# Kernel optimization log

Measured on AMD Instinct MI355X. Metric: run time of the kernel, lower is better.

Reference implementation:

```python
import jax, jax.numpy as jnp
import numpy as np

N = 100000   # nodes
E = 1200000  # edges
G = 512      # graphs in batch
H = 64       # hidden_dim
EED = 8      # edge_emb_dim
VOCABS = (120, 10, 7, 5, 2)
EDIMS = (64, 16, 8, 8, 4)
BN_EPS = 1e-5


def _lin(x, w, b):
    # torch nn.Linear: y = x @ W^T + b
    return x @ w.T + b


def setup_inputs() -> dict:
    key = jax.random.key(0)
    ks = iter(jax.random.split(key, 64))
    s = 0.02
    d = {}
    d["x"] = jax.random.randint(next(ks), (N, 5), 0, 120)
    d["edge_index"] = jax.random.randint(next(ks), (2, E), 0, N)
    d["edge_attr"] = jax.random.randint(next(ks), (E, 3), 0, 16)
    d["batch"] = jnp.sort(jax.random.randint(next(ks), (N,), 0, G))
    for i, (v, dd) in enumerate(zip(VOCABS, EDIMS)):
        d[f"emb{i}"] = jax.random.normal(next(ks), (v, dd), jnp.float32) * s
    d["proj_w"] = jax.random.normal(next(ks), (H, sum(EDIMS)), jnp.float32) * s
    d["proj_b"] = jnp.zeros((H,), jnp.float32)
    for i in (1, 2, 3):
        d[f"eemb{i}"] = jax.random.normal(next(ks), (16, EED), jnp.float32) * s
        d[f"lin_e{i}_w"] = jax.random.normal(next(ks), (H, EED), jnp.float32) * s
        d[f"lin_e{i}_b"] = jnp.zeros((H,), jnp.float32)
        d[f"eps{i}"] = jnp.zeros((), jnp.float32)
        d[f"mlp{i}_w1"] = jax.random.normal(next(ks), (H, H), jnp.float32) * s
        d[f"mlp{i}_b1"] = jnp.zeros((H,), jnp.float32)
        d[f"mlp{i}_w2"] = jax.random.normal(next(ks), (H, H), jnp.float32) * s
        d[f"mlp{i}_b2"] = jnp.zeros((H,), jnp.float32)
    d["bn_g"] = jnp.ones((H,), jnp.float32)
    d["bn_b"] = jnp.zeros((H,), jnp.float32)
    d["bn_rm"] = jnp.zeros((H,), jnp.float32)
    d["bn_rv"] = jnp.ones((H,), jnp.float32)
    d["gate_w"] = jax.random.normal(next(ks), (1, H), jnp.float32) * s
    d["gate_b"] = jnp.zeros((1,), jnp.float32)
    d["head_w1"] = jax.random.normal(next(ks), (128, H), jnp.float32) * s
    d["head_b1"] = jnp.zeros((128,), jnp.float32)
    d["head_w2"] = jax.random.normal(next(ks), (1, 128), jnp.float32) * s
    d["head_b2"] = jnp.zeros((1,), jnp.float32)
    return d


def reference(x, edge_index, edge_attr, batch,
              emb0, emb1, emb2, emb3, emb4, proj_w, proj_b,
              eemb1, lin_e1_w, lin_e1_b, eps1, mlp1_w1, mlp1_b1, mlp1_w2, mlp1_b2,
              eemb2, lin_e2_w, lin_e2_b, eps2, mlp2_w1, mlp2_b1, mlp2_w2, mlp2_b2,
              eemb3, lin_e3_w, lin_e3_b, eps3, mlp3_w1, mlp3_b1, mlp3_w2, mlp3_b2,
              bn_g, bn_b, bn_rm, bn_rv, gate_w, gate_b,
              head_w1, head_b1, head_w2, head_b2):
    # --- node embedding lookup (clamped per-table, as in torch) ---
    tabs = [emb0, emb1, emb2, emb3, emb4]
    feats = [t[jnp.clip(x[:, i], 0, t.shape[0] - 1)] for i, t in enumerate(tabs)]
    h = jnp.concatenate(feats, axis=-1)            # [N, 100]
    h = _lin(h, proj_w, proj_b)                    # [N, H]  (dropout = identity, eval)

    # --- edge hash, shared by all blocks ---
    eh = (edge_attr[:, 0] + 3 * edge_attr[:, 1] + 7 * edge_attr[:, 2]) % 16  # [E]
    src, dst = edge_index[0], edge_index[1]

    def gine(h, eemb, lw, lb, eps, w1, b1, w2, b2):
        # GINEConv: mlp((1+eps) x_i + sum_j relu(x_j + lin(e_ij)))
        e = _lin(eemb[eh], lw, lb)                        # [E, H]
        msg = jax.nn.relu(h[src] + e)                     # [E, H] gather + combine
        agg = jax.ops.segment_sum(msg, dst, num_segments=N)  # scatter-add to targets
        z = (1.0 + eps) * h + agg
        return _lin(jax.nn.relu(_lin(z, w1, b1)), w2, b2)

    h = jax.nn.relu(gine(h, eemb1, lin_e1_w, lin_e1_b, eps1, mlp1_w1, mlp1_b1, mlp1_w2, mlp1_b2))
    h = jax.nn.relu(gine(h, eemb2, lin_e2_w, lin_e2_b, eps2, mlp2_w1, mlp2_b1, mlp2_w2, mlp2_b2))
    h = jax.nn.relu(gine(h, eemb3, lin_e3_w, lin_e3_b, eps3, mlp3_w1, mlp3_b1, mlp3_w2, mlp3_b2))

    # BatchNorm1d (eval mode, running stats)
    h = (h - bn_rm) * jax.lax.rsqrt(bn_rv + BN_EPS) * bn_g + bn_b

    # AttentionalAggregation: segment softmax over gate, weighted segment sum
    gate = _lin(h, gate_w, gate_b)[:, 0]                  # [N]
    m = jax.ops.segment_max(gate, batch, num_segments=G)  # [G]
    w = jnp.exp(gate - m[batch])
    den = jax.ops.segment_sum(w, batch, num_segments=G) + 1e-16
    alpha = w / den[batch]                                # [N]
    graph = jax.ops.segment_sum(alpha[:, None] * h, batch, num_segments=G)  # [G, H]

    out = _lin(jax.nn.relu(_lin(graph, head_w1, head_b1)), head_w2, head_b2)  # [G, 1]
    return out[:, 0]
```

## Files before the change

kernel.cpp:

```cpp
#include <hip/hip_runtime.h>
#include <stdint.h>

#define N_NODES 100000
#define N_EDGES 1200000
#define N_GRAPH 512
#define HID 64

#define NBUCK 391
#define BCAP  4096
#define CHUNK 4096

#define PRE_W0  (144 * 64 + 3 * 1024 + 64 + NBUCK)
#define PRE_JOBS (PRE_W0 + 6 * 4096)

typedef __attribute__((ext_vector_type(8))) short bshort8;
typedef __attribute__((ext_vector_type(4))) float f32x4;

__device__ __forceinline__ unsigned short f2bf(float f) {
    unsigned u = __float_as_uint(f);
    u += 0x7FFF + ((u >> 16) & 1);
    return (unsigned short)(u >> 16);
}
__device__ __forceinline__ float bf2f(unsigned short b) {
    return __uint_as_float((unsigned)b << 16);
}

__global__ __launch_bounds__(256) void k_pre(
    const float* emb0, const float* emb1, const float* emb2, const float* emb3, const float* emb4,
    const float* proj_w,
    const float* ee1, const float* lw1, const float* lb1,
    const float* ee2, const float* lw2, const float* lb2,
    const float* ee3, const float* lw3, const float* lb3,
    const float* bn_g, const float* bn_b, const float* bn_rm, const float* bn_rv,
    const float* w11, const float* w12, const float* w21, const float* w22,
    const float* w31, const float* w32,
    float* ptab, float* elin, float* bnsc, float* bnsh, int* cursor,
    unsigned short* wbf)
{
    int job = blockIdx.x * 256 + threadIdx.x;
    if (job < 144 * 64) {
        int row = job >> 6, c = job & 63;
        const float* emb; int lr, dim, off;
        if (row < 120)      { emb = emb0; lr = row;       dim = 64; off = 0;  }
        else if (row < 130) { emb = emb1; lr = row - 120; dim = 16; off = 64; }
        else if (row < 137) { emb = emb2; lr = row - 130; dim = 8;  off = 80; }
        else if (row < 142) { emb = emb3; lr = row - 137; dim = 8;  off = 88; }
        else                { emb = emb4; lr = row - 142; dim = 4;  off = 96; }
        float s = 0.f;
        for (int d = 0; d < dim; ++d)
            s += emb[lr * dim + d] * proj_w[c * 100 + off + d];
        ptab[row * 64 + c] = s;
    } else if (job < 144 * 64 + 3 * 1024) {
        int j = job - 144 * 64;
        int L = j >> 10; int r = (j >> 6) & 15; int c = j & 63;
        const float* ee = (L == 0) ? ee1 : (L == 1) ? ee2 : ee3;
        const float* lw = (L == 0) ? lw1 : (L == 1) ? lw2 : lw3;
        const float* lb = (L == 0) ? lb1 : (L == 1) ? lb2 : lb3;
        float s = lb[c];
        for (int d = 0; d < 8; ++d) s += ee[r * 8 + d] * lw[c * 8 + d];
        elin[j] = s;
    } else if (job < 144 * 64 + 3 * 1024 + 64) {
        int c = job - (144 * 64 + 3 * 1024);
        float sc = bn_g[c] * rsqrtf(bn_rv[c] + 1e-5f);
        bnsc[c] = sc;
        bnsh[c] = bn_b[c] - bn_rm[c] * sc;
    } else if (job < PRE_W0) {
        cursor[job - (144 * 64 + 3 * 1024 + 64)] = 0;
    } else if (job < PRE_JOBS) {
        int j2 = job - PRE_W0;
        int sel = j2 >> 12;
        const float* W = (sel == 0) ? w11 : (sel == 1) ? w12 : (sel == 2) ? w21
                       : (sel == 3) ? w22 : (sel == 4) ? w31 : w32;
        wbf[j2] = f2bf(W[j2 & 4095]);
    }
}

__global__ __launch_bounds__(256) void k_embed(const int* x, const float* ptab,
                                               const float* proj_b, unsigned short* h2) {
    int id = blockIdx.x * 256 + threadIdx.x;
    if (id >= N_NODES * HID) return;
    int n = id >> 6, c = id & 63;
    const int* xr = x + n * 5;
    int r0 = min(max(xr[0], 0), 119);
    int r1 = 120 + min(max(xr[1], 0), 9);
    int r2 = 130 + min(max(xr[2], 0), 6);
    int r3 = 137 + min(max(xr[3], 0), 4);
    int r4 = 142 + min(max(xr[4], 0), 1);
    float v = proj_b[c] + ptab[r0 * 64 + c] + ptab[r1 * 64 + c] + ptab[r2 * 64 + c]
            + ptab[r3 * 64 + c] + ptab[r4 * 64 + c];
    h2[id] = f2bf(v);
}

__global__ __launch_bounds__(256) void k_gptr(const int* batch, int* gptr) {
    int n = blockIdx.x * 256 + threadIdx.x;
    if (n >= N_NODES) return;
    int b = batch[n];
    int bp = (n == 0) ? -1 : batch[n - 1];
    for (int g = bp + 1; g <= b; ++g) gptr[g] = n;
    if (n == N_NODES - 1) {
        for (int g = b + 1; g <= N_GRAPH; ++g) gptr[g] = N_NODES;
    }
}

__global__ __launch_bounds__(256) void k_bin(const int* __restrict__ ei,
                                             const int* __restrict__ ea,
                                             int* __restrict__ cursor,
                                             int* __restrict__ binned) {
    __shared__ int pay[CHUNK];
    __shared__ unsigned short bkid[CHUNK];
    __shared__ int hist[NBUCK], inc[NBUCK], tmp[NBUCK], gdelta[NBUCK];
    int t = threadIdx.x;
    int e0 = blockIdx.x * CHUNK;
    for (int i = t; i < NBUCK; i += 256) hist[i] = 0;
    __syncthreads();
    int mypay[16], myrb[16];
    #pragma unroll
    for (int j = 0; j < 16; ++j) {
        int e = e0 + j * 256 + t;
        myrb[j] = -1;
        if (e < N_EDGES) {
            int s = ei[e];
            int d = ei[N_EDGES + e];
            int hsh = (ea[e * 3] + 3 * ea[e * 3 + 1] + 7 * ea[e * 3 + 2]) & 15;
            int b = d >> 8;
            mypay[j] = s | (hsh << 17) | ((d & 255) << 21);
            int r = atomicAdd(&hist[b], 1);
            myrb[j] = r | (b << 12);
        }
    }
    __syncthreads();
    for (int i = t; i < NBUCK; i += 256) inc[i] = hist[i];
    __syncthreads();
    for (int off = 1; off < NBUCK; off <<= 1) {
        for (int i = t; i < NBUCK; i += 256) tmp[i] = inc[i] + ((i >= off) ? inc[i - off] : 0);
        __syncthreads();
        for (int i = t; i < NBUCK; i += 256) inc[i] = tmp[i];
        __syncthreads();
    }
    for (int i = t; i < NBUCK; i += 256) {
        int c = hist[i];
        int gp = c ? atomicAdd(&cursor[i], c) : 0;
        gdelta[i] = i * BCAP + gp - (inc[i] - c);
    }
    __syncthreads();
    #pragma unroll
    for (int j = 0; j < 16; ++j) {
        if (myrb[j] >= 0) {
            int b = myrb[j] >> 12, r = myrb[j] & 0xFFF;
            int slot = (inc[b] - hist[b]) + r;
            pay[slot] = mypay[j];
            bkid[slot] = (unsigned short)b;
        }
    }
    __syncthreads();
    int tot = inc[NBUCK - 1];
    for (int i = t; i < tot; i += 256)
        binned[gdelta[bkid[i]] + i] = pay[i];
}

__global__ __launch_bounds__(512) void k_bscan(const int* cursor, int* bbase, int* rowptr) {
    __shared__ int s[512], tp[512];
    int t = threadIdx.x;
    int v = (t < NBUCK) ? cursor[t] : 0;
    s[t] = v;
    __syncthreads();
    for (int off = 1; off < 512; off <<= 1) {
        tp[t] = s[t] + ((t >= off) ? s[t - off] : 0);
        __syncthreads();
        s[t] = tp[t];
        __syncthreads();
    }
    if (t < NBUCK) bbase[t] = s[t] - v;
    if (t == 0) { bbase[NBUCK] = N_EDGES; rowptr[N_NODES] = N_EDGES; }
}

__global__ __launch_bounds__(256) void k_fin(const int* __restrict__ binned,
                                             const int* __restrict__ cursor,
                                             const int* __restrict__ bbase,
                                             int* __restrict__ rowptr,
                                             int* __restrict__ epk) {
    __shared__ int h2[256], sc[256], cur[256];
    int b = blockIdx.x, t = threadIdx.x;
    int cnt = cursor[b];
    int gb = bbase[b];
    int node0 = b << 8;
    h2[t] = 0;
    __syncthreads();
    const int* bp = binned + b * BCAP;
    for (int i = t; i < cnt; i += 256) atomicAdd(&h2[(bp[i] >> 21) & 255], 1);
    __syncthreads();
    sc[t] = h2[t];
    __syncthreads();
    for (int off = 1; off < 256; off <<= 1) {
        int v = (t >= off) ? sc[t - off] : 0;
        __syncthreads();
        sc[t] += v;
        __syncthreads();
    }
    int ex = sc[t] - h2[t];
    cur[t] = ex;
    int n = node0 + t;
    if (n < N_NODES) rowptr[n] = gb + ex;
    __syncthreads();
    for (int i = t; i < cnt; i += 256) {
        int p = bp[i];
        int pos = atomicAdd(&cur[(p >> 21) & 255], 1);
        epk[gb + pos] = p & 0x1FFFFF;
    }
}

__global__ __launch_bounds__(256) void k_gather(const unsigned short* __restrict__ h2,
                                                const float* __restrict__ elinL,
                                                const int* __restrict__ rowptr,
                                                const int* __restrict__ epk,
                                                float* __restrict__ agg) {
    __shared__ float es[16 * 64];
    int t = threadIdx.x;
    ((float4*)es)[t] = ((const float4*)elinL)[t];
    __syncthreads();
    int n = blockIdx.x * 4 + (t >> 6);
    if (n >= N_NODES) return;
    int lane = t & 63;
    int grp = lane >> 4;
    int c4 = (lane & 15) << 2;
    int p0 = rowptr[n], p1 = rowptr[n + 1];
    int deg = p1 - p0;
    int nb = min(deg, 64);
    int pkv = (lane < deg) ? epk[p0 + lane] : 0;
    float4 acc = make_float4(0.f, 0.f, 0.f, 0.f);
    #pragma unroll
    for (int j = 0; j < 8; ++j) {
        int e = grp + j * 4;
        if (e < nb) {
            int pk = __shfl(pkv, e, 64);
            ushort4 a = *(const ushort4*)(h2 + (pk & 0x1FFFF) * 64 + c4);
            float4 ev = *(const float4*)(es + ((pk >> 17) & 15) * 64 + c4);
            acc.x += fmaxf(bf2f(a.x) + ev.x, 0.f);
            acc.y += fmaxf(bf2f(a.y) + ev.y, 0.f);
            acc.z += fmaxf(bf2f(a.z) + ev.z, 0.f);
            acc.w += fmaxf(bf2f(a.w) + ev.w, 0.f);
        }
    }
    for (int e = grp + 32; e < nb; e += 4) {
        int pk = __shfl(pkv, e, 64);
        ushort4 a = *(const ushort4*)(h2 + (pk & 0x1FFFF) * 64 + c4);
        float4 ev = *(const float4*)(es + ((pk >> 17) & 15) * 64 + c4);
        acc.x += fmaxf(bf2f(a.x) + ev.x, 0.f);
        acc.y += fmaxf(bf2f(a.y) + ev.y, 0.f);
        acc.z += fmaxf(bf2f(a.z) + ev.z, 0.f);
        acc.w += fmaxf(bf2f(a.w) + ev.w, 0.f);
    }
    for (int p = p0 + 64 + grp; p < p1; p += 4) {
        int pk = epk[p];
        ushort4 a = *(const ushort4*)(h2 + (pk & 0x1FFFF) * 64 + c4);
        float4 ev = *(const float4*)(es + ((pk >> 17) & 15) * 64 + c4);
        acc.x += fmaxf(bf2f(a.x) + ev.x, 0.f);
        acc.y += fmaxf(bf2f(a.y) + ev.y, 0.f);
        acc.z += fmaxf(bf2f(a.z) + ev.z, 0.f);
        acc.w += fmaxf(bf2f(a.w) + ev.w, 0.f);
    }
    acc.x += __shfl_down(acc.x, 32, 64);
    acc.y += __shfl_down(acc.y, 32, 64);
    acc.z += __shfl_down(acc.z, 32, 64);
    acc.w += __shfl_down(acc.w, 32, 64);
    acc.x += __shfl_down(acc.x, 16, 64);
    acc.y += __shfl_down(acc.y, 16, 64);
    acc.z += __shfl_down(acc.z, 16, 64);
    acc.w += __shfl_down(acc.w, 16, 64);
    if (grp == 0) *(float4*)(agg + n * 64 + c4) = acc;
}

__global__ __launch_bounds__(256) void k_mlpm(const unsigned short* __restrict__ h2in,
                                              const float* __restrict__ agg,
                                              const float* __restrict__ epsp,
                                              const unsigned short* __restrict__ wbf1,
                                              const float* __restrict__ b1,
                                              const unsigned short* __restrict__ wbf2,
                                              const float* __restrict__ b2,
                                              unsigned short* __restrict__ h2out,
                                              const float* __restrict__ bnsc,
                                              const float* __restrict__ bnsh,
                                              const float* __restrict__ gate_w,
                                              const float* __restrict__ gate_b,
                                              float* __restrict__ gate) {
    __shared__ unsigned short zb[64 * 72];
    __shared__ unsigned short hb[64 * 72];
    int t = threadIdx.x;
    int row0 = blockIdx.x * 64;
    float epsv = 1.f + epsp[0];
    for (int idx = t; idx < 1024; idx += 256) {
        int r = idx >> 4, c4 = (idx & 15) << 2;
        int gr = row0 + r;
        ushort4 zv = {0, 0, 0, 0};
        if (gr < N_NODES) {
            ushort4 a = *(const ushort4*)(h2in + gr * 64 + c4);
            float4 b = *(const float4*)(agg + gr * 64 + c4);
            zv.x = f2bf(epsv * bf2f(a.x) + b.x);
            zv.y = f2bf(epsv * bf2f(a.y) + b.y);
            zv.z = f2bf(epsv * bf2f(a.z) + b.z);
            zv.w = f2bf(epsv * bf2f(a.w) + b.w);
        }
        *(ushort4*)(zb + r * 72 + c4) = zv;
    }
    int lane = t & 63, wv = t >> 6;
    int quad = lane >> 4, lc = lane & 15;
    int m0 = wv * 16;
    bshort8 w1f[4][2];
    #pragma unroll
    for (int nt = 0; nt < 4; ++nt)
        #pragma unroll
        for (int kt = 0; kt < 2; ++kt)
            w1f[nt][kt] = *(const bshort8*)(wbf1 + (nt * 16 + lc) * 64 + kt * 32 + quad * 8);
    bshort8 w2f[4][2];
    #pragma unroll
    for (int nt = 0; nt < 4; ++nt)
        #pragma unroll
        for (int kt = 0; kt < 2; ++kt)
            w2f[nt][kt] = *(const bshort8*)(wbf2 + (nt * 16 + lc) * 64 + kt * 32 + quad * 8);
    __syncthreads();
    bshort8 a0 = *(const bshort8*)(zb + (m0 + lc) * 72 + quad * 8);
    bshort8 a1 = *(const bshort8*)(zb + (m0 + lc) * 72 + 32 + quad * 8);
    f32x4 acc1[4];
    #pragma unroll
    for (int nt = 0; nt < 4; ++nt) {
        acc1[nt] = (f32x4){0.f, 0.f, 0.f, 0.f};
        acc1[nt] = __builtin_amdgcn_mfma_f32_16x16x32_bf16(a0, w1f[nt][0], acc1[nt], 0, 0, 0);
        acc1[nt] = __builtin_amdgcn_mfma_f32_16x16x32_bf16(a1, w1f[nt][1], acc1[nt], 0, 0, 0);
    }
    #pragma unroll
    for (int nt = 0; nt < 4; ++nt) {
        float bb = b1[nt * 16 + lc];
        #pragma unroll
        for (int reg = 0; reg < 4; ++reg) {
            float v = fmaxf(acc1[nt][reg] + bb, 0.f);
            hb[(m0 + quad * 4 + reg) * 72 + nt * 16 + lc] = f2bf(v);
        }
    }
    bshort8 c0 = *(const bshort8*)(hb + (m0 + lc) * 72 + quad * 8);
    bshort8 c1 = *(const bshort8*)(hb + (m0 + lc) * 72 + 32 + quad * 8);
    f32x4 acc2[4];
    #pragma unroll
    for (int nt = 0; nt < 4; ++nt) {
        acc2[nt] = (f32x4){0.f, 0.f, 0.f, 0.f};
        acc2[nt] = __builtin_amdgcn_mfma_f32_16x16x32_bf16(c0, w2f[nt][0], acc2[nt], 0, 0, 0);
        acc2[nt] = __builtin_amdgcn_mfma_f32_16x16x32_bf16(c1, w2f[nt][1], acc2[nt], 0, 0, 0);
    }
    if (gate == nullptr) {
        #pragma unroll
        for (int reg = 0; reg < 4; ++reg) {
            int gr = row0 + m0 + quad * 4 + reg;
            if (gr < N_NODES) {
                #pragma unroll
                for (int nt = 0; nt < 4; ++nt) {
                    int col = nt * 16 + lc;
                    float v = fmaxf(acc2[nt][reg] + b2[col], 0.f);
                    h2out[gr * 64 + col] = f2bf(v);
                }
            }
        }
    } else {
        float gb = gate_b[0];
        #pragma unroll
        for (int reg = 0; reg < 4; ++reg) {
            int gr = row0 + m0 + quad * 4 + reg;
            float p = 0.f;
            #pragma unroll
            for (int nt = 0; nt < 4; ++nt) {
                int col = nt * 16 + lc;
                float v = fmaxf(acc2[nt][reg] + b2[col], 0.f) * bnsc[col] + bnsh[col];
                p += v * gate_w[col];
                if (gr < N_NODES) h2out[gr * 64 + col] = f2bf(v);
            }
            p += __shfl_down(p, 8, 16);
            p += __shfl_down(p, 4, 16);
            p += __shfl_down(p, 2, 16);
            p += __shfl_down(p, 1, 16);
            if (lc == 0 && gr < N_NODES) gate[gr] = p + gb;
        }
    }
}

__global__ __launch_bounds__(256) void k_att(const unsigned short* __restrict__ h2,
                                             const float* __restrict__ gate,
                                             const int* __restrict__ gptr,
                                             const float* __restrict__ hw1,
                                             const float* __restrict__ hb1,
                                             const float* __restrict__ hw2,
                                             const float* __restrict__ hb2,
                                             float* __restrict__ out) {
    __shared__ float red[4];
    __shared__ float acc_s[4][64];
    __shared__ float gvec[64];
    __shared__ float m_s, den_s;
    int t = threadIdx.x, g = blockIdx.x;
    int n0 = gptr[g], n1 = gptr[g + 1];
    float m = -INFINITY;
    for (int n = n0 + t; n < n1; n += 256) m = fmaxf(m, gate[n]);
    #pragma unroll
    for (int off = 32; off > 0; off >>= 1) m = fmaxf(m, __shfl_down(m, off, 64));
    if ((t & 63) == 0) red[t >> 6] = m;
    __syncthreads();
    if (t == 0) m_s = fmaxf(fmaxf(red[0], red[1]), fmaxf(red[2], red[3]));
    __syncthreads();
    m = m_s;
    float s = 0.f;
    for (int n = n0 + t; n < n1; n += 256) s += expf(gate[n] - m);
    #pragma unroll
    for (int off = 32; off > 0; off >>= 1) s += __shfl_down(s, off, 64);
    if ((t & 63) == 0) red[t >> 6] = s;
    __syncthreads();
    if (t == 0) den_s = red[0] + red[1] + red[2] + red[3] + 1e-16f;
    __syncthreads();
    float invden = 1.f / den_s;
    int c = t & 63, w = t >> 6;
    float acc = 0.f;
    for (int n = n0 + w; n < n1; n += 4) {
        float a = expf(gate[n] - m);
        acc += a * bf2f(h2[n * 64 + c]);
    }
    acc_s[w][c] = acc;
    __syncthreads();
    if (w == 0)
        gvec[c] = (acc_s[0][c] + acc_s[1][c] + acc_s[2][c] + acc_s[3][c]) * invden;
    __syncthreads();
    float p = 0.f;
    if (t < 128) {
        float sh = hb1[t];
        const float* wr = hw1 + t * 64;
        #pragma unroll
        for (int k = 0; k < 64; ++k) sh += gvec[k] * wr[k];
        p = fmaxf(sh, 0.f) * hw2[t];
    }
    #pragma unroll
    for (int off = 32; off > 0; off >>= 1) p += __shfl_down(p, off, 64);
    if (t == 0) red[0] = p;
    if (t == 64) red[1] = p;
    __syncthreads();
    if (t == 0) out[g] = red[0] + red[1] + hb2[0];
}

extern "C" void kernel_launch(void* const* d_in, const int* in_sizes, int n_in,
                              void* d_out, int out_size, void* d_ws, size_t ws_size,
                              hipStream_t stream) {
    const int* x    = (const int*)d_in[0];
    const int* ei   = (const int*)d_in[1];
    const int* ea   = (const int*)d_in[2];
    const int* bat  = (const int*)d_in[3];
    const float* emb0 = (const float*)d_in[4];
    const float* emb1 = (const float*)d_in[5];
    const float* emb2 = (const float*)d_in[6];
    const float* emb3 = (const float*)d_in[7];
    const float* emb4 = (const float*)d_in[8];
    const float* proj_w = (const float*)d_in[9];
    const float* proj_b = (const float*)d_in[10];
    const float* bn_g  = (const float*)d_in[35];
    const float* bn_b  = (const float*)d_in[36];
    const float* bn_rm = (const float*)d_in[37];
    const float* bn_rv = (const float*)d_in[38];
    const float* gate_w = (const float*)d_in[39];
    const float* gate_b = (const float*)d_in[40];
    const float* head_w1 = (const float*)d_in[41];
    const float* head_b1 = (const float*)d_in[42];
    const float* head_w2 = (const float*)d_in[43];
    const float* head_b2 = (const float*)d_in[44];

    char* wsb = (char*)d_ws;
    size_t o = 0;
    auto alloc = [&](size_t bytes) -> void* {
        void* p = wsb + o;
        o += (bytes + 255) & ~(size_t)255;
        return p;
    };
    float* ptab   = (float*)alloc(144 * 64 * 4);
    float* elin   = (float*)alloc(3 * 16 * 64 * 4);
    float* bnsc   = (float*)alloc(64 * 4);
    float* bnsh   = (float*)alloc(64 * 4);
    int* cursor   = (int*)alloc(NBUCK * 4);
    int* bbase    = (int*)alloc((NBUCK + 1) * 4);
    int* gptr     = (int*)alloc((N_GRAPH + 1) * 4);
    int* rowptr   = (int*)alloc(((size_t)N_NODES + 1) * 4);
    int* binned   = (int*)alloc((size_t)NBUCK * BCAP * 4);
    int* epk      = (int*)alloc((size_t)N_EDGES * 4);
    unsigned short* h2 = (unsigned short*)alloc((size_t)N_NODES * 64 * 2);
    float* agg    = (float*)alloc((size_t)N_NODES * 64 * 4);
    float* gate   = (float*)alloc((size_t)N_NODES * 4);
    unsigned short* wbf = (unsigned short*)alloc(6 * 4096 * 2);

    k_pre<<<(PRE_JOBS + 255) / 256, 256, 0, stream>>>(
                                  emb0, emb1, emb2, emb3, emb4, proj_w,
                                  (const float*)d_in[11], (const float*)d_in[12], (const float*)d_in[13],
                                  (const float*)d_in[19], (const float*)d_in[20], (const float*)d_in[21],
                                  (const float*)d_in[27], (const float*)d_in[28], (const float*)d_in[29],
                                  bn_g, bn_b, bn_rm, bn_rv,
                                  (const float*)d_in[15], (const float*)d_in[17],
                                  (const float*)d_in[23], (const float*)d_in[25],
                                  (const float*)d_in[31], (const float*)d_in[33],
                                  ptab, elin, bnsc, bnsh, cursor, wbf);
    k_embed<<<(N_NODES * 64 + 255) / 256, 256, 0, stream>>>(x, ptab, proj_b, h2);
    k_gptr<<<(N_NODES + 255) / 256, 256, 0, stream>>>(bat, gptr);
    k_bin<<<(N_EDGES + CHUNK - 1) / CHUNK, 256, 0, stream>>>(ei, ea, cursor, binned);
    k_bscan<<<1, 512, 0, stream>>>(cursor, bbase, rowptr);
    k_fin<<<NBUCK, 256, 0, stream>>>(binned, cursor, bbase, rowptr, epk);

    for (int L = 0; L < 3; ++L) {
        const float* epsp = (const float*)d_in[14 + L * 8];
        const float* b1   = (const float*)d_in[16 + L * 8];
        const float* b2   = (const float*)d_in[18 + L * 8];
        const unsigned short* wb1 = wbf + (L * 2 + 0) * 4096;
        const unsigned short* wb2 = wbf + (L * 2 + 1) * 4096;
        k_gather<<<(N_NODES + 3) / 4, 256, 0, stream>>>(h2, elin + L * 1024, rowptr, epk, agg);
        if (L < 2) {
            k_mlpm<<<(N_NODES + 63) / 64, 256, 0, stream>>>(h2, agg, epsp, wb1, b1, wb2, b2, h2,
                                                            nullptr, nullptr, nullptr, nullptr,
                                                            nullptr);
        } else {
            k_mlpm<<<(N_NODES + 63) / 64, 256, 0, stream>>>(h2, agg, epsp, wb1, b1, wb2, b2, h2,
                                                            bnsc, bnsh, gate_w, gate_b, gate);
        }
    }

    k_att<<<N_GRAPH, 256, 0, stream>>>(h2, gate, gptr, head_w1, head_b1, head_w2, head_b2,
                                       (float*)d_out);
}
```

Baseline: 439.3 us.

## Fuse edge gather-aggregate into MLP kernel with ping-pong node buffers

Measured after the change: 394.9 us. 1.11x faster.

```diff
diff --git a/kernel.cpp b/kernel.cpp
--- a/kernel.cpp
+++ b/kernel.cpp
@@ -209,69 +209,10 @@
     }
 }
 
-__global__ __launch_bounds__(256) void k_gather(const unsigned short* __restrict__ h2,
-                                                const float* __restrict__ elinL,
-                                                const int* __restrict__ rowptr,
-                                                const int* __restrict__ epk,
-                                                float* __restrict__ agg) {
-    __shared__ float es[16 * 64];
-    int t = threadIdx.x;
-    ((float4*)es)[t] = ((const float4*)elinL)[t];
-    __syncthreads();
-    int n = blockIdx.x * 4 + (t >> 6);
-    if (n >= N_NODES) return;
-    int lane = t & 63;
-    int grp = lane >> 4;
-    int c4 = (lane & 15) << 2;
-    int p0 = rowptr[n], p1 = rowptr[n + 1];
-    int deg = p1 - p0;
-    int nb = min(deg, 64);
-    int pkv = (lane < deg) ? epk[p0 + lane] : 0;
-    float4 acc = make_float4(0.f, 0.f, 0.f, 0.f);
-    #pragma unroll
-    for (int j = 0; j < 8; ++j) {
-        int e = grp + j * 4;
-        if (e < nb) {
-            int pk = __shfl(pkv, e, 64);
-            ushort4 a = *(const ushort4*)(h2 + (pk & 0x1FFFF) * 64 + c4);
-            float4 ev = *(const float4*)(es + ((pk >> 17) & 15) * 64 + c4);
-            acc.x += fmaxf(bf2f(a.x) + ev.x, 0.f);
-            acc.y += fmaxf(bf2f(a.y) + ev.y, 0.f);
-            acc.z += fmaxf(bf2f(a.z) + ev.z, 0.f);
-            acc.w += fmaxf(bf2f(a.w) + ev.w, 0.f);
-        }
-    }
-    for (int e = grp + 32; e < nb; e += 4) {
-        int pk = __shfl(pkv, e, 64);
-        ushort4 a = *(const ushort4*)(h2 + (pk & 0x1FFFF) * 64 + c4);
-        float4 ev = *(const float4*)(es + ((pk >> 17) & 15) * 64 + c4);
-        acc.x += fmaxf(bf2f(a.x) + ev.x, 0.f);
-        acc.y += fmaxf(bf2f(a.y) + ev.y, 0.f);
-        acc.z += fmaxf(bf2f(a.z) + ev.z, 0.f);
-        acc.w += fmaxf(bf2f(a.w) + ev.w, 0.f);
-    }
-    for (int p = p0 + 64 + grp; p < p1; p += 4) {
-        int pk = epk[p];
-        ushort4 a = *(const ushort4*)(h2 + (pk & 0x1FFFF) * 64 + c4);
-        float4 ev = *(const float4*)(es + ((pk >> 17) & 15) * 64 + c4);
-        acc.x += fmaxf(bf2f(a.x) + ev.x, 0.f);
-        acc.y += fmaxf(bf2f(a.y) + ev.y, 0.f);
-        acc.z += fmaxf(bf2f(a.z) + ev.z, 0.f);
-        acc.w += fmaxf(bf2f(a.w) + ev.w, 0.f);
-    }
-    acc.x += __shfl_down(acc.x, 32, 64);
-    acc.y += __shfl_down(acc.y, 32, 64);
-    acc.z += __shfl_down(acc.z, 32, 64);
-    acc.w += __shfl_down(acc.w, 32, 64);
-    acc.x += __shfl_down(acc.x, 16, 64);
-    acc.y += __shfl_down(acc.y, 16, 64);
-    acc.z += __shfl_down(acc.z, 16, 64);
-    acc.w += __shfl_down(acc.w, 16, 64);
-    if (grp == 0) *(float4*)(agg + n * 64 + c4) = acc;
-}
-
-__global__ __launch_bounds__(256) void k_mlpm(const unsigned short* __restrict__ h2in,
-                                              const float* __restrict__ agg,
+__global__ __launch_bounds__(256) void k_gmlp(const unsigned short* __restrict__ h2in,
+                                              const float* __restrict__ elinL,
+                                              const int* __restrict__ rowptr,
+                                              const int* __restrict__ epk,
                                               const float* __restrict__ epsp,
                                               const unsigned short* __restrict__ wbf1,
                                               const float* __restrict__ b1,
@@ -283,41 +224,86 @@
                                               const float* __restrict__ gate_w,
                                               const float* __restrict__ gate_b,
                                               float* __restrict__ gate) {
+    __shared__ float es[16 * 64];
     __shared__ unsigned short zb[64 * 72];
     __shared__ unsigned short hb[64 * 72];
     int t = threadIdx.x;
+    ((float4*)es)[t] = ((const float4*)elinL)[t];
+    __syncthreads();
     int row0 = blockIdx.x * 64;
+    int lane = t & 63, wv = t >> 6;
+    int grp = lane >> 4, lc = lane & 15;
+    int c4 = lc << 2;
+    int m0 = wv * 16;
     float epsv = 1.f + epsp[0];
-    for (int idx = t; idx < 1024; idx += 256) {
-        int r = idx >> 4, c4 = (idx & 15) << 2;
-        int gr = row0 + r;
-        ushort4 zv = {0, 0, 0, 0};
-        if (gr < N_NODES) {
-            ushort4 a = *(const ushort4*)(h2in + gr * 64 + c4);
-            float4 b = *(const float4*)(agg + gr * 64 + c4);
-            zv.x = f2bf(epsv * bf2f(a.x) + b.x);
-            zv.y = f2bf(epsv * bf2f(a.y) + b.y);
-            zv.z = f2bf(epsv * bf2f(a.z) + b.z);
-            zv.w = f2bf(epsv * bf2f(a.w) + b.w);
-        }
-        *(ushort4*)(zb + r * 72 + c4) = zv;
-    }
-    int lane = t & 63, wv = t >> 6;
-    int quad = lane >> 4, lc = lane & 15;
-    int m0 = wv * 16;
-    bshort8 w1f[4][2];
+    for (int i = 0; i < 16; ++i) {
+        int n = row0 + m0 + i;
+        float4 acc = make_float4(0.f, 0.f, 0.f, 0.f);
+        ushort4 hs = {0, 0, 0, 0};
+        if (n < N_NODES) {
+            int p0 = rowptr[n], p1 = rowptr[n + 1];
+            int deg = p1 - p0;
+            hs = *(const ushort4*)(h2in + n * 64 + c4);
+            int nb = min(deg, 64);
+            int pkv = (lane < deg) ? epk[p0 + lane] : 0;
+            #pragma unroll
+            for (int j = 0; j < 8; ++j) {
+                int e = grp + j * 4;
+                if (e < nb) {
+                    int pk = __shfl(pkv, e, 64);
+                    ushort4 a = *(const ushort4*)(h2in + (pk & 0x1FFFF) * 64 + c4);
+                    float4 ev = *(const float4*)(es + ((pk >> 17) & 15) * 64 + c4);
+                    acc.x += fmaxf(bf2f(a.x) + ev.x, 0.f);
+                    acc.y += fmaxf(bf2f(a.y) + ev.y, 0.f);
+                    acc.z += fmaxf(bf2f(a.z) + ev.z, 0.f);
+                    acc.w += fmaxf(bf2f(a.w) + ev.w, 0.f);
+                }
+            }
+            for (int e = grp + 32; e < nb; e += 4) {
+                int pk = __shfl(pkv, e, 64);
+                ushort4 a = *(const ushort4*)(h2in + (pk & 0x1FFFF) * 64 + c4);
+                float4 ev = *(const float4*)(es + ((pk >> 17) & 15) * 64 + c4);
+                acc.x += fmaxf(bf2f(a.x) + ev.x, 0.f);
+                acc.y += fmaxf(bf2f(a.y) + ev.y, 0.f);
+                acc.z += fmaxf(bf2f(a.z) + ev.z, 0.f);
+                acc.w += fmaxf(bf2f(a.w) + ev.w, 0.f);
+            }
+            for (int p = p0 + 64 + grp; p < p1; p += 4) {
+                int pk = epk[p];
+                ushort4 a = *(const ushort4*)(h2in + (pk & 0x1FFFF) * 64 + c4);
+                float4 ev = *(const float4*)(es + ((pk >> 17) & 15) * 64 + c4);
+                acc.x += fmaxf(bf2f(a.x) + ev.x, 0.f);
+                acc.y += fmaxf(bf2f(a.y) + ev.y, 0.f);
+                acc.z += fmaxf(bf2f(a.z) + ev.z, 0.f);
+                acc.w += fmaxf(bf2f(a.w) + ev.w, 0.f);
+            }
+        }
+        acc.x += __shfl_down(acc.x, 32, 64);
+        acc.y += __shfl_down(acc.y, 32, 64);
+        acc.z += __shfl_down(acc.z, 32, 64);
+        acc.w += __shfl_down(acc.w, 32, 64);
+        acc.x += __shfl_down(acc.x, 16, 64);
+        acc.y += __shfl_down(acc.y, 16, 64);
+        acc.z += __shfl_down(acc.z, 16, 64);
+        acc.w += __shfl_down(acc.w, 16, 64);
+        if (grp == 0) {
+            ushort4 zv;
+            zv.x = f2bf(epsv * bf2f(hs.x) + acc.x);
+            zv.y = f2bf(epsv * bf2f(hs.y) + acc.y);
+            zv.z = f2bf(epsv * bf2f(hs.z) + acc.z);
+            zv.w = f2bf(epsv * bf2f(hs.w) + acc.w);
+            *(ushort4*)(zb + (m0 + i) * 72 + c4) = zv;
+        }
+    }
+    int quad = grp;
+    bshort8 w1f[4][2], w2f[4][2];
     #pragma unroll
     for (int nt = 0; nt < 4; ++nt)
         #pragma unroll
-        for (int kt = 0; kt < 2; ++kt)
+        for (int kt = 0; kt < 2; ++kt) {
             w1f[nt][kt] = *(const bshort8*)(wbf1 + (nt * 16 + lc) * 64 + kt * 32 + quad * 8);
-    bshort8 w2f[4][2];
-    #pragma unroll
-    for (int nt = 0; nt < 4; ++nt)
-        #pragma unroll
-        for (int kt = 0; kt < 2; ++kt)
             w2f[nt][kt] = *(const bshort8*)(wbf2 + (nt * 16 + lc) * 64 + kt * 32 + quad * 8);
-    __syncthreads();
+        }
     bshort8 a0 = *(const bshort8*)(zb + (m0 + lc) * 72 + quad * 8);
     bshort8 a1 = *(const bshort8*)(zb + (m0 + lc) * 72 + 32 + quad * 8);
     f32x4 acc1[4];
@@ -481,8 +467,8 @@
     int* rowptr   = (int*)alloc(((size_t)N_NODES + 1) * 4);
     int* binned   = (int*)alloc((size_t)NBUCK * BCAP * 4);
     int* epk      = (int*)alloc((size_t)N_EDGES * 4);
-    unsigned short* h2 = (unsigned short*)alloc((size_t)N_NODES * 64 * 2);
-    float* agg    = (float*)alloc((size_t)N_NODES * 64 * 4);
+    unsigned short* h2a = (unsigned short*)alloc((size_t)N_NODES * 64 * 2);
+    unsigned short* h2b = (unsigned short*)alloc((size_t)N_NODES * 64 * 2);
     float* gate   = (float*)alloc((size_t)N_NODES * 4);
     unsigned short* wbf = (unsigned short*)alloc(6 * 4096 * 2);
 
@@ -496,29 +482,33 @@
                                   (const float*)d_in[23], (const float*)d_in[25],
                                   (const float*)d_in[31], (const float*)d_in[33],
                                   ptab, elin, bnsc, bnsh, cursor, wbf);
-    k_embed<<<(N_NODES * 64 + 255) / 256, 256, 0, stream>>>(x, ptab, proj_b, h2);
+    k_embed<<<(N_NODES * 64 + 255) / 256, 256, 0, stream>>>(x, ptab, proj_b, h2a);
     k_gptr<<<(N_NODES + 255) / 256, 256, 0, stream>>>(bat, gptr);
     k_bin<<<(N_EDGES + CHUNK - 1) / CHUNK, 256, 0, stream>>>(ei, ea, cursor, binned);
     k_bscan<<<1, 512, 0, stream>>>(cursor, bbase, rowptr);
     k_fin<<<NBUCK, 256, 0, stream>>>(binned, cursor, bbase, rowptr, epk);
 
+    unsigned short* hin = h2a;
+    unsigned short* hout = h2b;
     for (int L = 0; L < 3; ++L) {
         const float* epsp = (const float*)d_in[14 + L * 8];
         const float* b1   = (const float*)d_in[16 + L * 8];
         const float* b2   = (const float*)d_in[18 + L * 8];
         const unsigned short* wb1 = wbf + (L * 2 + 0) * 4096;
         const unsigned short* wb2 = wbf + (L * 2 + 1) * 4096;
-        k_gather<<<(N_NODES + 3) / 4, 256, 0, stream>>>(h2, elin + L * 1024, rowptr, epk, agg);
         if (L < 2) {
-            k_mlpm<<<(N_NODES + 63) / 64, 256, 0, stream>>>(h2, agg, epsp, wb1, b1, wb2, b2, h2,
+            k_gmlp<<<(N_NODES + 63) / 64, 256, 0, stream>>>(hin, elin + L * 1024, rowptr, epk,
+                                                            epsp, wb1, b1, wb2, b2, hout,
                                                             nullptr, nullptr, nullptr, nullptr,
                                                             nullptr);
         } else {
-            k_mlpm<<<(N_NODES + 63) / 64, 256, 0, stream>>>(h2, agg, epsp, wb1, b1, wb2, b2, h2,
+            k_gmlp<<<(N_NODES + 63) / 64, 256, 0, stream>>>(hin, elin + L * 1024, rowptr, epk,
+                                                            epsp, wb1, b1, wb2, b2, hout,
                                                             bnsc, bnsh, gate_w, gate_b, gate);
         }
-    }
-
-    k_att<<<N_GRAPH, 256, 0, stream>>>(h2, gate, gptr, head_w1, head_b1, head_w2, head_b2,
+        unsigned short* tmp = hin; hin = hout; hout = tmp;
+    }
+
+    k_att<<<N_GRAPH, 256, 0, stream>>>(hin, gate, gptr, head_w1, head_b1, head_w2, head_b2,
                                        (float*)d_out);
 }
```
